# Kernel optimization log

Measured on AMD Instinct MI355X. Metric: run time of the kernel, lower is better.

Reference implementation:

```python
import jax, jax.numpy as jnp
import numpy as np

HEADS = 4
DIM_HEAD = 64
DIM = 256
FMAP = 64
SCALE = DIM_HEAD ** -0.5


def setup_inputs() -> dict:
    key = jax.random.key(0)
    k1, k2, k3, k4 = jax.random.split(key, 4)
    inner = HEADS * DIM_HEAD
    fmap = jax.random.normal(k1, (4, DIM, FMAP, FMAP), dtype=jnp.float32)
    # 1x1 conv weight for qkv projection: (3*inner_dim, dim)
    w_qkv = jax.random.normal(k2, (3 * inner, DIM), dtype=jnp.float32) * (DIM ** -0.5)
    # AbsPosEmb parameters, initialized as randn * dim_head**-0.5 (as in BoTNet)
    pos_height = jax.random.normal(k3, (FMAP, DIM_HEAD), dtype=jnp.float32) * SCALE
    pos_width = jax.random.normal(k4, (FMAP, DIM_HEAD), dtype=jnp.float32) * SCALE
    return {"fmap": fmap, "w_qkv": w_qkv, "pos_height": pos_height, "pos_width": pos_width}


def reference(fmap, w_qkv, pos_height, pos_width):
    b, c, h, w = fmap.shape
    hw = h * w
    # 1x1 conv (no bias) == channel matmul
    qkv = jnp.einsum('bchw,oc->bohw', fmap, w_qkv)  # (b, 3*inner, h, w)
    q, k, v = jnp.split(qkv, 3, axis=1)
    # replicate torch .view(b, heads, h*w, -1): raw row-major reshape
    q = q.reshape(b, HEADS, hw, DIM_HEAD) * SCALE
    k = k.reshape(b, HEADS, hw, DIM_HEAD)
    v = v.reshape(b, HEADS, hw, DIM_HEAD)
    sim = jnp.einsum('bhid,bhjd->bhij', q, k)  # (b, heads, hw, hw)
    # absolute positional bias: emb[j] = height[y] + width[x], j = y*w + x
    emb = (pos_height[:, None, :] + pos_width[None, :, :]).reshape(hw, DIM_HEAD)
    sim = sim + jnp.einsum('bhid,jd->bhij', q, emb)
    attn = jax.nn.softmax(sim, axis=-1)
    out = jnp.einsum('bhij,bhjd->bhid', attn, v)  # (b, heads, hw, dim_head)
    # replicate torch .view(b, heads*dim_head, h, w): raw reshape
    return out.reshape(b, HEADS * DIM_HEAD, h, w)
```

## Files before the change

kernel.cpp:

```cpp
#include <hip/hip_runtime.h>


typedef float  f32x4  __attribute__((ext_vector_type(4)));
typedef __bf16 bf16x8 __attribute__((ext_vector_type(8)));
typedef __bf16 bf16x4 __attribute__((ext_vector_type(4)));

__device__ inline float fast_exp2(float x) {
#if __has_builtin(__builtin_amdgcn_exp2f)
  return __builtin_amdgcn_exp2f(x);
#else
  return exp2f(x);
#endif
}

__device__ inline void glds16(const __bf16* g, __bf16* l) {
  __builtin_amdgcn_global_load_lds(
      (const __attribute__((address_space(1))) void*)g,
      (__attribute__((address_space(3))) void*)l, 16, 0, 0);
}

__global__ __launch_bounds__(256) void w_cvt(
    const float* __restrict__ w, __bf16* __restrict__ wb)
{
  int idx = blockIdx.x * 256 + threadIdx.x;
  f32x4 v = ((const f32x4*)w)[idx];
  bf16x4 o; o[0]=(__bf16)v[0]; o[1]=(__bf16)v[1]; o[2]=(__bf16)v[2]; o[3]=(__bf16)v[3];
  ((bf16x4*)wb)[idx] = o;
}

__global__ __launch_bounds__(256) void qkv_proj(
    const float* __restrict__ fmap, const __bf16* __restrict__ wb,
    const float* __restrict__ ph,   const float* __restrict__ pw,
    __bf16* __restrict__ Qw, __bf16* __restrict__ Kw, __bf16* __restrict__ Vw)
{
  constexpr int LS = 264;
  __shared__ __bf16 Bs[32 * LS];
  const int tid  = threadIdx.x;
  const int wv   = tid >> 6;
  const int lane = tid & 63;
  const int quad = lane >> 4, l15 = lane & 15;
  const int n0 = blockIdx.x * 32;
  const int b  = blockIdx.y;

#pragma unroll
  for (int i = 0; i < 2; ++i) {
    int id = tid + i * 256;
    int ng = id & 7;
    int kg = id >> 3;
    const float* base = fmap + ((size_t)b * 256 + 4 * kg) * 4096 + n0 + 4 * ng;
    f32x4 v0 = *(const f32x4*)(base);
    f32x4 v1 = *(const f32x4*)(base + 4096);
    f32x4 v2 = *(const f32x4*)(base + 8192);
    f32x4 v3 = *(const f32x4*)(base + 12288);
#pragma unroll
    for (int j = 0; j < 4; ++j) {
      bf16x4 o; o[0]=(__bf16)v0[j]; o[1]=(__bf16)v1[j]; o[2]=(__bf16)v2[j]; o[3]=(__bf16)v3[j];
      *(bf16x4*)(&Bs[(4 * ng + j) * LS + 4 * kg]) = o;
    }
  }
  __syncthreads();

  for (int mt = 0; mt < 12; ++mt) {
    const int region = mt >> 2;
    const int obase  = (mt & 3) * 64;
    const __bf16* aptr = wb + (size_t)(mt * 64 + 16 * wv + l15) * 256 + 8 * quad;

    f32x4 acc[2] = {};
#pragma unroll
    for (int k0 = 0; k0 < 256; k0 += 32) {
      bf16x8 af = *(const bf16x8*)(aptr + k0);
      bf16x8 b0 = *(const bf16x8*)(&Bs[(l15)      * LS + k0 + 8 * quad]);
      bf16x8 b1 = *(const bf16x8*)(&Bs[(16 + l15) * LS + k0 + 8 * quad]);
      acc[0] = __builtin_amdgcn_mfma_f32_16x16x32_bf16(af, b0, acc[0], 0, 0, 0);
      acc[1] = __builtin_amdgcn_mfma_f32_16x16x32_bf16(af, b1, acc[1], 0, 0, 0);
    }

#pragma unroll
    for (int t = 0; t < 2; ++t) {
#pragma unroll
      for (int rr = 0; rr < 4; ++rr) {
        int oreg = obase + 16 * wv + 4 * quad + rr;
        int s    = n0 + 16 * t + l15;
        float val = acc[t][rr];
        size_t off = ((size_t)(b * 256 + oreg)) * 4096 + s;
        if (region == 0) {
          Qw[off] = (__bf16)(val * 0.18033688f);
        } else if (region == 1) {
          int g = oreg & 63;
          float bias = ph[g * 64 + (s & 63)] + pw[(s >> 6) * 64 + (s & 63)];
          Kw[off] = (__bf16)(val + bias);
        } else {
          Vw[off] = (__bf16)val;
        }
      }
    }
  }
}

__global__ __launch_bounds__(256) void v_transpose(
    const __bf16* __restrict__ Vw, __bf16* __restrict__ Vt)
{
  __shared__ __bf16 T[64 * 72];
  const int tid = threadIdx.x;
  const int j0  = blockIdx.x * 64;
  const int bh  = blockIdx.y;
  const __bf16* src = Vw + (size_t)bh * 262144;
#pragma unroll
  for (int i = 0; i < 2; ++i) {
    int id = tid + i * 256;
    int r = id >> 3, c = (id & 7) * 8;
    *(bf16x8*)(&T[r * 72 + c]) = *(const bf16x8*)(src + (size_t)(j0 + r) * 64 + c);
  }
  __syncthreads();
#pragma unroll
  for (int i = 0; i < 2; ++i) {
    int id = tid + i * 256;
    int d = id >> 3, jc = (id & 7) * 8;
    bf16x8 o;
#pragma unroll
    for (int z = 0; z < 8; ++z) o[z] = T[(jc + z) * 72 + d];
    *(bf16x8*)(Vt + ((size_t)bh * 64 + d) * 4096 + j0 + jc) = o;
  }
}

__global__ __launch_bounds__(512, 2) void flash_attn(
    const __bf16* __restrict__ Qg, const __bf16* __restrict__ Kg,
    const __bf16* __restrict__ Vtg, float* __restrict__ out)
{
  __shared__ __align__(16) __bf16 SMEM[65536];
  __bf16* Ks = SMEM;
  __bf16* Vs = SMEM + 32768;

  const int tid  = threadIdx.x;
  const int wv   = tid >> 6;
  const int lane = tid & 63;
  const int quad = lane >> 4, l15 = lane & 15;
  const int zi   = wv >> 2;
  const int wl   = wv & 3;
  const int bh = blockIdx.y;
  const int iw = blockIdx.x * 256 + 64 * wl;
  const __bf16* Qb = Qg  + (size_t)bh * 262144;
  const __bf16* Kb = Kg  + (size_t)bh * 262144;
  const __bf16* Vb = Vtg + (size_t)bh * 262144;

  bf16x8 qf[4][2];
#pragma unroll
  for (int m = 0; m < 4; ++m)
#pragma unroll
    for (int c = 0; c < 2; ++c)
      qf[m][c] = *(const bf16x8*)(Qb + (size_t)(iw + 16 * m + l15) * 64 + 32 * c + 8 * quad);

  const int r0  = tid >> 3;
  const int kch = tid & 7;
  const int xc  = (kch ^ (r0 & 7)) * 8;
  const int prr = (r0 & 0x23) | ((r0 & 0x0C) << 1) | ((r0 & 0x10) >> 2);
  const __bf16* kp0 = Kb + (size_t)prr * 64 + xc;
  const __bf16* kp1 = Kb + (size_t)(2048 + prr) * 64 + xc;
  const __bf16* vp0 = Vb + (size_t)r0 * 4096 + xc;
  const __bf16* vp1 = Vb + (size_t)r0 * 4096 + 2048 + xc;

  f32x4 acco[4][4] = {};
  f32x4 lacc[4] = {};
  const int swz = (l15 & 7);

  bf16x8 onesb;
#pragma unroll
  for (int r = 0; r < 8; ++r) onesb[r] = (__bf16)1.0f;

  auto dma_tile = [&](int buf) {
    __bf16* kd0 = &Ks[buf * 8192 + tid * 8];
    __bf16* kd1 = &Ks[16384 + buf * 8192 + tid * 8];
    __bf16* vd0 = &Vs[buf * 8192 + tid * 8];
    __bf16* vd1 = &Vs[16384 + buf * 8192 + tid * 8];
    glds16(kp0, kd0);         kp0 += 4096;
    glds16(kp0, kd0 + 4096);  kp0 += 4096;
    glds16(kp1, kd1);         kp1 += 4096;
    glds16(kp1, kd1 + 4096);  kp1 += 4096;
    glds16(vp0, vd0);         vp0 += 64;
    glds16(vp0, vd0 + 4096);  vp0 += 64;
    glds16(vp1, vd1);         vp1 += 64;
    glds16(vp1, vd1 + 4096);  vp1 += 64;
  };

  auto compute_tile = [&](int buf, int sub) {
    const __bf16* Kbuf = &Ks[zi * 16384 + buf * 8192 + sub * 4096];
    const __bf16* Vbuf = &Vs[zi * 16384 + buf * 8192 + sub * 4096];
    f32x4 sacc[4][4] = {};
    __builtin_amdgcn_s_setprio(1);
#pragma unroll
    for (int c = 0; c < 2; ++c) {
#pragma unroll
      for (int t = 0; t < 4; ++t) {
        bf16x8 ak = *(const bf16x8*)(&Kbuf[(16 * t + l15) * 64 + (((4 * c + quad) ^ swz) * 8)]);
#pragma unroll
        for (int m = 0; m < 4; ++m)
          sacc[m][t] = __builtin_amdgcn_mfma_f32_16x16x32_bf16(ak, qf[m][c], sacc[m][t], 0, 0, 0);
      }
    }
    __builtin_amdgcn_s_setprio(0);
    bf16x8 pf[4][2];
#pragma unroll
    for (int m = 0; m < 4; ++m) {
#pragma unroll
      for (int t = 0; t < 4; ++t)
#pragma unroll
        for (int r = 0; r < 4; ++r)
          sacc[m][t][r] = fast_exp2(sacc[m][t][r]);
#pragma unroll
      for (int c2 = 0; c2 < 2; ++c2) {
        bf16x8 a;
#pragma unroll
        for (int r = 0; r < 4; ++r) {
          a[r]     = (__bf16)sacc[m][2 * c2][r];
          a[4 + r] = (__bf16)sacc[m][2 * c2 + 1][r];
        }
        pf[m][c2] = a;
      }
    }
    __builtin_amdgcn_s_setprio(1);
#pragma unroll
    for (int c2 = 0; c2 < 2; ++c2) {
#pragma unroll
      for (int t = 0; t < 4; ++t) {
        bf16x8 bv = *(const bf16x8*)(&Vbuf[(16 * t + l15) * 64 + (((4 * c2 + quad) ^ swz) * 8)]);
#pragma unroll
        for (int m = 0; m < 4; ++m)
          acco[m][t] = __builtin_amdgcn_mfma_f32_16x16x32_bf16(pf[m][c2], bv, acco[m][t], 0, 0, 0);
      }
#pragma unroll
      for (int m = 0; m < 4; ++m)
        lacc[m] = __builtin_amdgcn_mfma_f32_16x16x32_bf16(pf[m][c2], onesb, lacc[m], 0, 0, 0);
    }
    __builtin_amdgcn_s_setprio(0);
  };

  dma_tile(0);
  for (int it = 0; it < 16; it += 2) {
    __syncthreads();
    dma_tile(1);
    compute_tile(0, 0);
    compute_tile(0, 1);
    __syncthreads();
    if (it < 14) dma_tile(0);
    compute_tile(1, 0);
    compute_tile(1, 1);
  }

  __syncthreads();
  float* X = (float*)SMEM;
  const int slot = (wl * 64 + lane) * 84;
  if (zi == 1) {
#pragma unroll
    for (int m = 0; m < 4; ++m) {
#pragma unroll
      for (int t = 0; t < 4; ++t)
        *(f32x4*)(&X[slot + m * 16 + t * 4]) = acco[m][t];
      *(f32x4*)(&X[slot + 64 + m * 4]) = lacc[m];
    }
  }
  __syncthreads();
  if (zi == 0) {
    float* Ob = out + (size_t)bh * 262144;
#pragma unroll
    for (int m = 0; m < 4; ++m) {
      f32x4 l1 = *(const f32x4*)(&X[slot + 64 + m * 4]);
      f32x4 lt = lacc[m] + l1;
      f32x4 inv;
#pragma unroll
      for (int r = 0; r < 4; ++r) inv[r] = 1.0f / lt[r];
#pragma unroll
      for (int t = 0; t < 4; ++t) {
        f32x4 o1 = *(const f32x4*)(&X[slot + m * 16 + t * 4]);
        f32x4 ot = acco[m][t] + o1;
#pragma unroll
        for (int r = 0; r < 4; ++r)
          Ob[(size_t)(iw + 16 * m + 4 * quad + r) * 64 + 16 * t + l15] =
              ot[r] * inv[r];
      }
    }
  }
}

extern "C" void kernel_launch(void* const* d_in, const int* in_sizes, int n_in,
                              void* d_out, int out_size, void* d_ws, size_t ws_size,
                              hipStream_t stream) {
  const float* fmap = (const float*)d_in[0];
  const float* w    = (const float*)d_in[1];
  const float* ph   = (const float*)d_in[2];
  const float* pw   = (const float*)d_in[3];
  float* out = (float*)d_out;

  __bf16* Qw = (__bf16*)d_ws;
  __bf16* Kw = Qw + 4194304;
  __bf16* Vw = Kw + 4194304;
  __bf16* Vt = Vw + 4194304;
  __bf16* Wb16 = Vt + 4194304;

  w_cvt      <<<dim3(192),    256, 0, stream>>>(w, Wb16);
  qkv_proj   <<<dim3(128, 4), 256, 0, stream>>>(fmap, Wb16, ph, pw, Qw, Kw, Vw);
  v_transpose<<<dim3(64, 16), 256, 0, stream>>>(Vw, Vt);
  flash_attn <<<dim3(16, 16), 512, 0, stream>>>(Qw, Kw, Vt, out);
}
```

Measured before the change: 170.7 us.

## Fuse V transpose into flash attention via register-staged transposed LDS writes

Removes the separate v_transpose kernel and its workspace buffer. The attention kernel now loads untransposed V rows into registers, issuing the loads before compute so they overlap it, then scatters them transposed and swizzled into LDS after compute. This drops one kernel launch and a full read/write pass over V. In exchange it adds register pressure and many scalar 2-byte LDS stores, which may cause bank conflicts, in place of the async global-to-LDS DMA for V.

Result: slower. 278.9 us (+63.4%).

```diff
diff --git a/kernel.cpp b/kernel.cpp
--- a/kernel.cpp
+++ b/kernel.cpp
@@ -97,35 +97,9 @@
   }
 }
 
-__global__ __launch_bounds__(256) void v_transpose(
-    const __bf16* __restrict__ Vw, __bf16* __restrict__ Vt)
-{
-  __shared__ __bf16 T[64 * 72];
-  const int tid = threadIdx.x;
-  const int j0  = blockIdx.x * 64;
-  const int bh  = blockIdx.y;
-  const __bf16* src = Vw + (size_t)bh * 262144;
-#pragma unroll
-  for (int i = 0; i < 2; ++i) {
-    int id = tid + i * 256;
-    int r = id >> 3, c = (id & 7) * 8;
-    *(bf16x8*)(&T[r * 72 + c]) = *(const bf16x8*)(src + (size_t)(j0 + r) * 64 + c);
-  }
-  __syncthreads();
-#pragma unroll
-  for (int i = 0; i < 2; ++i) {
-    int id = tid + i * 256;
-    int d = id >> 3, jc = (id & 7) * 8;
-    bf16x8 o;
-#pragma unroll
-    for (int z = 0; z < 8; ++z) o[z] = T[(jc + z) * 72 + d];
-    *(bf16x8*)(Vt + ((size_t)bh * 64 + d) * 4096 + j0 + jc) = o;
-  }
-}
-
 __global__ __launch_bounds__(512, 2) void flash_attn(
     const __bf16* __restrict__ Qg, const __bf16* __restrict__ Kg,
-    const __bf16* __restrict__ Vtg, float* __restrict__ out)
+    const __bf16* __restrict__ Vg, float* __restrict__ out)
 {
   __shared__ __align__(16) __bf16 SMEM[65536];
   __bf16* Ks = SMEM;
@@ -139,9 +113,9 @@
   const int wl   = wv & 3;
   const int bh = blockIdx.y;
   const int iw = blockIdx.x * 256 + 64 * wl;
-  const __bf16* Qb = Qg  + (size_t)bh * 262144;
-  const __bf16* Kb = Kg  + (size_t)bh * 262144;
-  const __bf16* Vb = Vtg + (size_t)bh * 262144;
+  const __bf16* Qb = Qg + (size_t)bh * 262144;
+  const __bf16* Kb = Kg + (size_t)bh * 262144;
+  const __bf16* Vb = Vg + (size_t)bh * 262144;
 
   bf16x8 qf[4][2];
 #pragma unroll
@@ -156,8 +130,9 @@
   const int prr = (r0 & 0x23) | ((r0 & 0x0C) << 1) | ((r0 & 0x10) >> 2);
   const __bf16* kp0 = Kb + (size_t)prr * 64 + xc;
   const __bf16* kp1 = Kb + (size_t)(2048 + prr) * 64 + xc;
-  const __bf16* vp0 = Vb + (size_t)r0 * 4096 + xc;
-  const __bf16* vp1 = Vb + (size_t)r0 * 4096 + 2048 + xc;
+
+  const int jv  = tid >> 3;
+  const int d0v = (tid & 7) * 8;
 
   f32x4 acco[4][4] = {};
   f32x4 lacc[4] = {};
@@ -167,19 +142,36 @@
 #pragma unroll
   for (int r = 0; r < 8; ++r) onesb[r] = (__bf16)1.0f;
 
-  auto dma_tile = [&](int buf) {
+  auto dma_k = [&](int buf) {
     __bf16* kd0 = &Ks[buf * 8192 + tid * 8];
     __bf16* kd1 = &Ks[16384 + buf * 8192 + tid * 8];
-    __bf16* vd0 = &Vs[buf * 8192 + tid * 8];
-    __bf16* vd1 = &Vs[16384 + buf * 8192 + tid * 8];
     glds16(kp0, kd0);         kp0 += 4096;
     glds16(kp0, kd0 + 4096);  kp0 += 4096;
     glds16(kp1, kd1);         kp1 += 4096;
     glds16(kp1, kd1 + 4096);  kp1 += 4096;
-    glds16(vp0, vd0);         vp0 += 64;
-    glds16(vp0, vd0 + 4096);  vp0 += 64;
-    glds16(vp1, vd1);         vp1 += 64;
-    glds16(vp1, vd1 + 4096);  vp1 += 64;
+  };
+
+  auto v_loads = [&](int tj, bf16x8* vr) {
+#pragma unroll
+    for (int i = 0; i < 4; ++i) {
+      int zl = i >> 1, sub = i & 1;
+      vr[i] = *(const bf16x8*)(Vb + (size_t)(zl * 2048 + tj + sub * 64 + jv) * 64 + d0v);
+    }
+  };
+
+  auto v_writes = [&](int buf, const bf16x8* vr) {
+    const int jlow = jv & 7;
+    const int jgrp = jv >> 3;
+#pragma unroll
+    for (int i = 0; i < 4; ++i) {
+      int zl = i >> 1, sub = i & 1;
+      __bf16* base = &Vs[zl * 16384 + buf * 8192 + sub * 4096];
+#pragma unroll
+      for (int k = 0; k < 8; ++k) {
+        int d = d0v + k;
+        base[d * 64 + ((jgrp ^ k) * 8) + jlow] = vr[i][k];
+      }
+    }
   };
 
   auto compute_tile = [&](int buf, int sub) {
@@ -234,16 +226,26 @@
     __builtin_amdgcn_s_setprio(0);
   };
 
-  dma_tile(0);
+  bf16x8 vreg[4];
+  int tj = 0;
+  dma_k(0);
+  v_loads(tj, vreg); tj += 128;
+  v_writes(0, vreg);
   for (int it = 0; it < 16; it += 2) {
     __syncthreads();
-    dma_tile(1);
+    dma_k(1);
+    v_loads(tj, vreg); tj += 128;
     compute_tile(0, 0);
     compute_tile(0, 1);
+    v_writes(1, vreg);
     __syncthreads();
-    if (it < 14) dma_tile(0);
+    if (it < 14) {
+      dma_k(0);
+      v_loads(tj, vreg); tj += 128;
+    }
     compute_tile(1, 0);
     compute_tile(1, 1);
+    if (it < 14) v_writes(0, vreg);
   }
 
   __syncthreads();
@@ -293,11 +295,9 @@
   __bf16* Qw = (__bf16*)d_ws;
   __bf16* Kw = Qw + 4194304;
   __bf16* Vw = Kw + 4194304;
-  __bf16* Vt = Vw + 4194304;
-  __bf16* Wb16 = Vt + 4194304;
-
-  w_cvt      <<<dim3(192),    256, 0, stream>>>(w, Wb16);
-  qkv_proj   <<<dim3(128, 4), 256, 0, stream>>>(fmap, Wb16, ph, pw, Qw, Kw, Vw);
-  v_transpose<<<dim3(64, 16), 256, 0, stream>>>(Vw, Vt);
-  flash_attn <<<dim3(16, 16), 512, 0, stream>>>(Qw, Kw, Vt, out);
-}
+  __bf16* Wb16 = Vw + 4194304;
+
+  w_cvt    <<<dim3(192),    256, 0, stream>>>(w, Wb16);
+  qkv_proj <<<dim3(128, 4), 256, 0, stream>>>(fmap, Wb16, ph, pw, Qw, Kw, Vw);
+  flash_attn<<<dim3(16, 16), 512, 0, stream>>>(Qw, Kw, Vw, out);
+}
```
